# Kernel optimization log

Hardware: AMD Instinct MI355X
Metric: run time of the kernel (lower is better)

## Reference

```python
import jax, jax.numpy as jnp
import numpy as np

N, D, C = 8192, 1024, 1000
T_SCALE = 0.3
LAM2 = 0.1


def setup_inputs() -> dict:
    key = jax.random.key(0)
    k1, k2, k3 = jax.random.split(key, 3)
    feat = jax.random.normal(k1, (N, D), dtype=jnp.float32)
    W = jax.random.normal(k2, (C, D), dtype=jnp.float32) * 0.02
    b = jnp.zeros((C,), dtype=jnp.float32)
    labels = jax.random.randint(k3, (N,), 0, C)
    return {"feat": feat, "labels": labels, "W": W, "b": b}


def _scl_loss(feat_n, labels, t):
    # feat_n: l2-normalized features [N, D]
    n = feat_n.shape[0]
    sim = (feat_n @ feat_n.T) / t                      # [N, N]
    eye = jnp.eye(n, dtype=bool)
    # denominator: sum_{k != i} exp(sim[i,k])  (log-domain, same math)
    bottom_log = jax.nn.logsumexp(jnp.where(eye, -jnp.inf, sim), axis=1)  # [N]
    # positive mask: same label, j != i
    pos = (labels[:, None] == labels[None, :]) & ~eye  # [N, N]
    counts = pos.sum(axis=1)                           # [N]
    # log(exp(sim_ij)/bottom_i) = sim_ij - bottom_log_i
    sum_log = jnp.sum(jnp.where(pos, sim - bottom_log[:, None], 0.0), axis=1)
    valid = counts > 0
    per_sample = jnp.where(valid, -sum_log / jnp.maximum(counts, 1), 0.0)
    n_valid = valid.sum()
    return jnp.where(n_valid > 0, per_sample.sum() / jnp.maximum(n_valid, 1), 0.0)


def reference(feat, labels, W, b):
    logits = feat @ W.T + b                            # [N, C]
    # cross entropy (mean over batch)
    logp = jax.nn.log_softmax(logits, axis=-1)
    ce = -jnp.mean(jnp.take_along_axis(logp, labels[:, None], axis=1)[:, 0])
    # supervised contrastive loss on l2-normalized features
    feat_n = feat / jnp.linalg.norm(feat, axis=1, keepdims=True)
    scl = _scl_loss(feat_n, labels, T_SCALE)
    loss = (1.0 - LAM2) * ce + LAM2 * scl
    return logits, loss
```

## Files before the change

### kernel.cpp

```cpp
#include <hip/hip_runtime.h>
#include <hip/hip_bf16.h>
#include <math.h>

#define N 8192
#define D 1024
#define C 1000
#define CP 1024
#define INV_T (1.0f / 0.3f)
#define SIM_SCALE (INV_T / 256.0f)

typedef __bf16 bf16_t;
typedef bf16_t bf16x8 __attribute__((ext_vector_type(8)));
typedef float f32x4 __attribute__((ext_vector_type(4)));

typedef __attribute__((address_space(3))) uint32_t lds_u32_t;
typedef const __attribute__((address_space(1))) uint32_t glb_u32_t;

#define ZBYTES (3 * N * 4 + 16)
#define NZB 25

__global__ void prep_kernel(const float* __restrict__ feat,
                            const float* __restrict__ W,
                            float* __restrict__ norms, bf16_t* __restrict__ feat_n,
                            unsigned int* __restrict__ feat_f8,
                            bf16_t* __restrict__ Wp, char* __restrict__ zbase) {
  int g = blockIdx.x;
  int t = threadIdx.x;
  if (g < N) {
    int row = g;
    const float4* fr = (const float4*)(feat + (size_t)row * D);
    float4 x = fr[t];
    float ss = x.x * x.x + x.y * x.y + x.z * x.z + x.w * x.w;
    for (int off = 32; off; off >>= 1) ss += __shfl_down(ss, off, 64);
    __shared__ float sred[4];
    __shared__ float srn;
    int lane = t & 63, w = t >> 6;
    if (lane == 0) sred[w] = ss;
    __syncthreads();
    if (t == 0) {
      float tot = sred[0] + sred[1] + sred[2] + sred[3];
      float nrm = sqrtf(tot);
      norms[row] = nrm;
      srn = 1.0f / nrm;
    }
    __syncthreads();
    float rn = srn;
    union { bf16_t h[4]; uint2 u; } pk;
    pk.h[0] = (bf16_t)(x.x * rn);
    pk.h[1] = (bf16_t)(x.y * rn);
    pk.h[2] = (bf16_t)(x.z * rn);
    pk.h[3] = (bf16_t)(x.w * rn);
    *(uint2*)(feat_n + (size_t)row * D + t * 4) = pk.u;
    float rs = rn * 16.0f;
    unsigned int u8 = 0;
    u8 = __builtin_amdgcn_cvt_pk_fp8_f32(x.x * rs, x.y * rs, u8, false);
    u8 = __builtin_amdgcn_cvt_pk_fp8_f32(x.z * rs, x.w * rs, u8, true);
    feat_f8[(size_t)row * 256 + t] = u8;
  } else if (g < N + CP) {
    int row = g - N;
    union { bf16_t h[4]; uint2 u; } pk;
    if (row < C) {
      float4 x = ((const float4*)(W + (size_t)row * D))[t];
      pk.h[0] = (bf16_t)x.x; pk.h[1] = (bf16_t)x.y;
      pk.h[2] = (bf16_t)x.z; pk.h[3] = (bf16_t)x.w;
    } else {
      pk.h[0] = pk.h[1] = pk.h[2] = pk.h[3] = (bf16_t)0.0f;
    }
    *(uint2*)(Wp + (size_t)row * D + t * 4) = pk.u;
  } else {
    size_t off = (size_t)(g - N - CP) * 4096 + (size_t)t * 16;
    if (off < (size_t)ZBYTES) {
      int4 z = {0, 0, 0, 0};
      *(int4*)(zbase + off) = z;
    }
  }
}

#define BM 128
#define BN 128
#define BK 64
#define NSIM 2080

__device__ __forceinline__ void stage_tile_bf16(const bf16_t* __restrict__ g0,
                                                bf16_t* lds, int t, int w) {
#pragma unroll
  for (int p = 0; p < 4; p++) {
    int chunk = p * 256 + t;
    int r = chunk >> 3;
    int c = (chunk & 7) ^ (r & 7);
    const bf16_t* gp = g0 + (size_t)r * D + c * 8;
    bf16_t* lp = lds + (size_t)(p * 256 + w * 64) * 8;
    __builtin_amdgcn_global_load_lds((glb_u32_t*)gp, (lds_u32_t*)lp, 16, 0, 0);
  }
}

__device__ __forceinline__ void stage_tile_f8(const unsigned char* __restrict__ g0,
                                              unsigned char* lds, int t, int w) {
#pragma unroll
  for (int p = 0; p < 2; p++) {
    int chunk = p * 256 + t;
    int r = chunk >> 2;
    int c = (chunk & 3) ^ ((r >> 1) & 3);
    const unsigned char* gp = g0 + (size_t)r * D + c * 16;
    unsigned char* lp = lds + (size_t)(p * 256 + w * 64) * 16;
    __builtin_amdgcn_global_load_lds((glb_u32_t*)gp, (lds_u32_t*)lp, 16, 0, 0);
  }
}

__launch_bounds__(256)
__global__ void logits_gemm(const bf16_t* __restrict__ A, const bf16_t* __restrict__ Wp,
                            const float* __restrict__ norms, const float* __restrict__ bias,
                            float* __restrict__ ceS, float* __restrict__ out) {
  __shared__ __align__(16) bf16_t As[BM * BK];
  __shared__ __align__(16) bf16_t Bs[BN * BK];
  int tileM = blockIdx.x * BM;
  int tileN = blockIdx.y * BN;
  int t = threadIdx.x;
  int lane = t & 63;
  int w = t >> 6;
  int wm = (w & 1) << 6;
  int wn = (w >> 1) << 6;
  int l15 = lane & 15;
  int quad = lane >> 4;
  f32x4 acc[4][4] = {};
  const bf16_t* Abase = A + (size_t)tileM * D;
  const bf16_t* Bbase = Wp + (size_t)tileN * D;

  for (int k0 = 0; k0 < D; k0 += BK) {
    stage_tile_bf16(Abase + k0, As, t, w);
    stage_tile_bf16(Bbase + k0, Bs, t, w);
    __syncthreads();
#pragma unroll
    for (int h = 0; h < 2; h++) {
      bf16x8 af[4], bfr[4];
#pragma unroll
      for (int i = 0; i < 4; i++) {
        int ar = wm + i * 16 + l15;
        int cc = (h * 4 + quad) ^ (ar & 7);
        af[i] = *(const bf16x8*)(&As[ar * BK + cc * 8]);
      }
#pragma unroll
      for (int j = 0; j < 4; j++) {
        int br = wn + j * 16 + l15;
        int cc = (h * 4 + quad) ^ (br & 7);
        bfr[j] = *(const bf16x8*)(&Bs[br * BK + cc * 8]);
      }
#pragma unroll
      for (int i = 0; i < 4; i++)
#pragma unroll
        for (int j = 0; j < 4; j++)
          acc[i][j] = __builtin_amdgcn_mfma_f32_16x16x32_bf16(af[i], bfr[j], acc[i][j], 0, 0, 0);
    }
    __syncthreads();
  }
#pragma unroll
  for (int i = 0; i < 4; i++) {
#pragma unroll
    for (int r = 0; r < 4; r++) {
      int gr = tileM + wm + i * 16 + quad * 4 + r;
      float nrm = norms[gr];
      float esum = 0.0f;
#pragma unroll
      for (int j = 0; j < 4; j++) {
        int gc = tileN + wn + j * 16 + l15;
        if (gc < C) {
          float lg = nrm * acc[i][j][r] + bias[gc];
          out[(size_t)gr * C + gc] = lg;
          esum += __expf(lg);
        }
      }
      for (int m = 1; m < 16; m <<= 1) esum += __shfl_xor(esum, m, 64);
      if (l15 == 0) atomicAdd(&ceS[gr], esum);
    }
  }
}

__launch_bounds__(256)
__global__ void sim_gemm(const unsigned char* __restrict__ A8, const int* __restrict__ labels,
                         float* __restrict__ S, float* __restrict__ P) {
  __shared__ __align__(16) unsigned char As[BM * 64];
  __shared__ __align__(16) unsigned char Bs[BN * 64];
  int g = blockIdx.x;
  int t = threadIdx.x;
  int lane = t & 63;
  int w = t >> 6;
  int wm = (w & 1) << 6;
  int wn = (w >> 1) << 6;
  int l15 = lane & 15;
  int quad = lane >> 4;
  f32x4 acc[4][4] = {};

  const int nb = N / BM;
  float fnb = (float)nb + 0.5f;
  int bi = (int)(fnb - sqrtf(fnb * fnb - 2.0f * (float)g));
  if (bi < 0) bi = 0;
#define TRI_OFF(r) ((r) * nb - (r) * ((r)-1) / 2)
  while (TRI_OFF(bi + 1) <= g) bi++;
  while (TRI_OFF(bi) > g) bi--;
  int bj = bi + (g - TRI_OFF(bi));
#undef TRI_OFF
  bi = __builtin_amdgcn_readfirstlane(bi);
  bj = __builtin_amdgcn_readfirstlane(bj);
  int tileM = bi * BM;
  int tileN = bj * BN;
  bool diag = (bi == bj);

  const unsigned char* Abase = A8 + (size_t)tileM * D;
  const unsigned char* Bbase = A8 + (size_t)tileN * D;

  for (int k0 = 0; k0 < D; k0 += BK) {
    stage_tile_f8(Abase + k0, As, t, w);
    stage_tile_f8(Bbase + k0, Bs, t, w);
    __syncthreads();
#pragma unroll
    for (int h = 0; h < 2; h++) {
      long af[4], bfr[4];
#pragma unroll
      for (int i = 0; i < 4; i++) {
        int ar = wm + i * 16 + l15;
        int c8 = h * 4 + quad;
        int boff = ((c8 >> 1) ^ ((ar >> 1) & 3)) * 16 + (c8 & 1) * 8;
        af[i] = *(const long*)(&As[ar * 64 + boff]);
      }
#pragma unroll
      for (int j = 0; j < 4; j++) {
        int br = wn + j * 16 + l15;
        int c8 = h * 4 + quad;
        int boff = ((c8 >> 1) ^ ((br >> 1) & 3)) * 16 + (c8 & 1) * 8;
        bfr[j] = *(const long*)(&Bs[br * 64 + boff]);
      }
#pragma unroll
      for (int i = 0; i < 4; i++)
#pragma unroll
        for (int j = 0; j < 4; j++)
          acc[i][j] = __builtin_amdgcn_mfma_f32_16x16x32_fp8_fp8(af[i], bfr[j], acc[i][j], 0, 0, 0);
    }
    __syncthreads();
  }

  int gcj[4], lc[4];
#pragma unroll
  for (int j = 0; j < 4; j++) {
    gcj[j] = tileN + wn + j * 16 + l15;
    lc[j] = labels[gcj[j]];
  }
  float csS[4] = {0.f, 0.f, 0.f, 0.f}, csP[4] = {0.f, 0.f, 0.f, 0.f};
#pragma unroll
  for (int i = 0; i < 4; i++) {
#pragma unroll
    for (int r = 0; r < 4; r++) {
      int gr = tileM + wm + i * 16 + quad * 4 + r;
      int lr = labels[gr];
      float ssum = 0.0f, psum = 0.0f;
#pragma unroll
      for (int j = 0; j < 4; j++) {
        float sim = acc[i][j][r] * SIM_SCALE;
        if (gcj[j] != gr) {
          float e = __expf(sim);
          float pv = (lc[j] == lr) ? sim : 0.0f;
          ssum += e;
          psum += pv;
          csS[j] += e;
          csP[j] += pv;
        }
      }
      for (int m = 1; m < 16; m <<= 1) {
        ssum += __shfl_xor(ssum, m, 64);
        psum += __shfl_xor(psum, m, 64);
      }
      if (l15 == 0) {
        atomicAdd(&S[gr], ssum);
        atomicAdd(&P[gr], psum);
      }
    }
  }
  if (!diag) {
#pragma unroll
    for (int j = 0; j < 4; j++) {
      csS[j] += __shfl_xor(csS[j], 16, 64);
      csS[j] += __shfl_xor(csS[j], 32, 64);
      csP[j] += __shfl_xor(csP[j], 16, 64);
      csP[j] += __shfl_xor(csP[j], 32, 64);
      if (quad == 0) {
        atomicAdd(&S[gcj[j]], csS[j]);
        atomicAdd(&P[gcj[j]], csP[j]);
      }
    }
  }
}

__global__ void final_kernel(const float* __restrict__ S, const float* __restrict__ P,
                             const int* __restrict__ labels,
                             const float* __restrict__ ceS, float* __restrict__ out,
                             float* __restrict__ accums) {
  __shared__ int lh[1024];
  int t = threadIdx.x;
  for (int i = t; i < 1024; i += 256) lh[i] = 0;
  __syncthreads();
  for (int i = t; i < N; i += 256) atomicAdd(&lh[labels[i]], 1);
  __syncthreads();

  int i = blockIdx.x * 256 + t;
  int lab = labels[i];
  float cesum = logf(ceS[i]) - out[(size_t)i * C + lab];
  float lsum = 0.0f, lval = 0.0f;
  int cnt = lh[lab] - 1;
  if (cnt > 0) {
    float bl = logf(S[i]);
    lsum = -(P[i] - (float)cnt * bl) / (float)cnt;
    lval = 1.0f;
  }
  for (int off = 32; off; off >>= 1) {
    cesum += __shfl_down(cesum, off, 64);
    lsum += __shfl_down(lsum, off, 64);
    lval += __shfl_down(lval, off, 64);
  }
  __shared__ float sc[4], ss[4], sv[4];
  int lane = t & 63, w = t >> 6;
  if (lane == 0) { sc[w] = cesum; ss[w] = lsum; sv[w] = lval; }
  __syncthreads();
  if (t == 0) {
    atomicAdd(&accums[0], sc[0] + sc[1] + sc[2] + sc[3]);
    atomicAdd(&accums[1], ss[0] + ss[1] + ss[2] + ss[3]);
    atomicAdd(&accums[2], sv[0] + sv[1] + sv[2] + sv[3]);
    __threadfence();
    unsigned int prev = atomicAdd((unsigned int*)&accums[3], 1u);
    if (prev == 31) {
      float a0 = atomicAdd(&accums[0], 0.0f);
      float a1 = atomicAdd(&accums[1], 0.0f);
      float a2 = atomicAdd(&accums[2], 0.0f);
      float ce = a0 * (1.0f / (float)N);
      float scl = (a2 > 0.0f) ? a1 / a2 : 0.0f;
      out[(size_t)N * C] = 0.9f * ce + 0.1f * scl;
    }
  }
}

extern "C" void kernel_launch(void* const* d_in, const int* in_sizes, int n_in,
                              void* d_out, int out_size, void* d_ws, size_t ws_size,
                              hipStream_t stream) {
  const float* feat   = (const float*)d_in[0];
  const int*   labels = (const int*)d_in[1];
  const float* W      = (const float*)d_in[2];
  const float* b      = (const float*)d_in[3];
  float* out = (float*)d_out;

  char* ws = (char*)d_ws;
  bf16_t*       feat_n  = (bf16_t*)ws;
  bf16_t*       Wp      = (bf16_t*)(ws + (size_t)N * D * 2);
  unsigned int* feat_f8 = (unsigned int*)(ws + (size_t)N * D * 2 + (size_t)CP * D * 2);
  float*  norms  = (float*)((char*)feat_f8 + (size_t)N * D);
  float*  S      = norms + N;
  float*  P      = S + N;
  float*  ceS    = P + N;
  float*  accums = ceS + N;

  prep_kernel<<<N + CP + NZB, 256, 0, stream>>>(feat, W, norms, feat_n, feat_f8,
                                                Wp, (char*)S);
  logits_gemm<<<dim3(N / BM, CP / BN), 256, 0, stream>>>(feat_n, Wp, norms, b, ceS, out);
  sim_gemm<<<NSIM, 256, 0, stream>>>((const unsigned char*)feat_f8, labels, S, P);
  final_kernel<<<N / 256, 256, 0, stream>>>(S, P, labels, ceS, out, accums);
}
```

Baseline: 248.8 us.

## Switch sim GEMM to 32x32x64 scaled FP8 MFMA and cache labels in LDS

Replaces the 16x16x32 FP8 MFMA tiling in the similarity GEMM with the gfx950 32x32x64 scaled f8f6f4 MFMA (unit scales). Fragments become 32-byte reads and the epilogue is remapped to the 32x32 accumulator layout. Tile labels are now staged into LDS once instead of read from global memory per row. The aim is fewer MFMA issues and fewer LDS reads per K step. In exchange, the row reductions now need 5-step shuffles and the new output row mapping must be exactly right.

```diff
diff --git a/kernel.cpp b/kernel.cpp
--- a/kernel.cpp
+++ b/kernel.cpp
@@ -12,6 +12,9 @@
 typedef __bf16 bf16_t;
 typedef bf16_t bf16x8 __attribute__((ext_vector_type(8)));
 typedef float f32x4 __attribute__((ext_vector_type(4)));
+typedef float f32x16 __attribute__((ext_vector_type(16)));
+typedef int v8i __attribute__((ext_vector_type(8)));
+typedef int v4i __attribute__((ext_vector_type(4)));
 
 typedef __attribute__((address_space(3))) uint32_t lds_u32_t;
 typedef const __attribute__((address_space(1))) uint32_t glb_u32_t;
@@ -107,6 +110,13 @@
   }
 }
 
+__device__ __forceinline__ v8i read_frag_f8(const unsigned char* rowbase, int s, int kh) {
+  v8i r;
+  *(v4i*)&r         = *(const v4i*)(rowbase + (((2 * kh) ^ s) << 4));
+  *(((v4i*)&r) + 1) = *(const v4i*)(rowbase + (((2 * kh + 1) ^ s) << 4));
+  return r;
+}
+
 __launch_bounds__(256)
 __global__ void logits_gemm(const bf16_t* __restrict__ A, const bf16_t* __restrict__ Wp,
                             const float* __restrict__ norms, const float* __restrict__ bias,
@@ -180,15 +190,17 @@
                          float* __restrict__ S, float* __restrict__ P) {
   __shared__ __align__(16) unsigned char As[BM * 64];
   __shared__ __align__(16) unsigned char Bs[BN * 64];
+  __shared__ int lblA[BM];
+  __shared__ int lblB[BN];
   int g = blockIdx.x;
   int t = threadIdx.x;
   int lane = t & 63;
   int w = t >> 6;
   int wm = (w & 1) << 6;
   int wn = (w >> 1) << 6;
-  int l15 = lane & 15;
-  int quad = lane >> 4;
-  f32x4 acc[4][4] = {};
+  int l31 = lane & 31;
+  int kh = lane >> 5;
+  f32x16 acc[2][2] = {};
 
   const int nb = N / BM;
   float fnb = (float)nb + 0.5f;
@@ -205,6 +217,9 @@
   int tileN = bj * BN;
   bool diag = (bi == bj);
 
+  if (t < BM) lblA[t] = labels[tileM + t];
+  else lblB[t - BM] = labels[tileN + (t - BM)];
+
   const unsigned char* Abase = A8 + (size_t)tileM * D;
   const unsigned char* Bbase = A8 + (size_t)tileN * D;
 
@@ -212,63 +227,59 @@
     stage_tile_f8(Abase + k0, As, t, w);
     stage_tile_f8(Bbase + k0, Bs, t, w);
     __syncthreads();
-#pragma unroll
-    for (int h = 0; h < 2; h++) {
-      long af[4], bfr[4];
-#pragma unroll
-      for (int i = 0; i < 4; i++) {
-        int ar = wm + i * 16 + l15;
-        int c8 = h * 4 + quad;
-        int boff = ((c8 >> 1) ^ ((ar >> 1) & 3)) * 16 + (c8 & 1) * 8;
-        af[i] = *(const long*)(&As[ar * 64 + boff]);
-      }
-#pragma unroll
-      for (int j = 0; j < 4; j++) {
-        int br = wn + j * 16 + l15;
-        int c8 = h * 4 + quad;
-        int boff = ((c8 >> 1) ^ ((br >> 1) & 3)) * 16 + (c8 & 1) * 8;
-        bfr[j] = *(const long*)(&Bs[br * 64 + boff]);
-      }
-#pragma unroll
-      for (int i = 0; i < 4; i++)
-#pragma unroll
-        for (int j = 0; j < 4; j++)
-          acc[i][j] = __builtin_amdgcn_mfma_f32_16x16x32_fp8_fp8(af[i], bfr[j], acc[i][j], 0, 0, 0);
-    }
-    __syncthreads();
-  }
-
-  int gcj[4], lc[4];
-#pragma unroll
-  for (int j = 0; j < 4; j++) {
-    gcj[j] = tileN + wn + j * 16 + l15;
-    lc[j] = labels[gcj[j]];
-  }
-  float csS[4] = {0.f, 0.f, 0.f, 0.f}, csP[4] = {0.f, 0.f, 0.f, 0.f};
-#pragma unroll
-  for (int i = 0; i < 4; i++) {
-#pragma unroll
-    for (int r = 0; r < 4; r++) {
-      int gr = tileM + wm + i * 16 + quad * 4 + r;
-      int lr = labels[gr];
+    v8i af[2], bf[2];
+#pragma unroll
+    for (int i = 0; i < 2; i++) {
+      int ar = wm + i * 32 + l31;
+      af[i] = read_frag_f8(&As[ar * 64], (ar >> 1) & 3, kh);
+    }
+#pragma unroll
+    for (int j = 0; j < 2; j++) {
+      int br = wn + j * 32 + l31;
+      bf[j] = read_frag_f8(&Bs[br * 64], (br >> 1) & 3, kh);
+    }
+#pragma unroll
+    for (int i = 0; i < 2; i++)
+#pragma unroll
+      for (int j = 0; j < 2; j++)
+        acc[i][j] = __builtin_amdgcn_mfma_scale_f32_32x32x64_f8f6f4(
+            af[i], bf[j], acc[i][j], 0, 0,
+            0, 0x7f7f7f7f, 0, 0x7f7f7f7f);
+    __syncthreads();
+  }
+
+  int gcj[2], lcj[2];
+#pragma unroll
+  for (int j = 0; j < 2; j++) {
+    gcj[j] = tileN + wn + j * 32 + l31;
+    lcj[j] = lblB[wn + j * 32 + l31];
+  }
+  float csS[2] = {0.f, 0.f}, csP[2] = {0.f, 0.f};
+#pragma unroll
+  for (int i = 0; i < 2; i++) {
+#pragma unroll
+    for (int reg = 0; reg < 16; reg++) {
+      int rrow = (reg & 3) + 8 * (reg >> 2) + 4 * kh;
+      int gr = tileM + wm + i * 32 + rrow;
+      int lr = lblA[wm + i * 32 + rrow];
       float ssum = 0.0f, psum = 0.0f;
 #pragma unroll
-      for (int j = 0; j < 4; j++) {
-        float sim = acc[i][j][r] * SIM_SCALE;
+      for (int j = 0; j < 2; j++) {
+        float sim = acc[i][j][reg] * SIM_SCALE;
         if (gcj[j] != gr) {
           float e = __expf(sim);
-          float pv = (lc[j] == lr) ? sim : 0.0f;
+          float pv = (lcj[j] == lr) ? sim : 0.0f;
           ssum += e;
           psum += pv;
           csS[j] += e;
           csP[j] += pv;
         }
       }
-      for (int m = 1; m < 16; m <<= 1) {
+      for (int m = 1; m < 32; m <<= 1) {
         ssum += __shfl_xor(ssum, m, 64);
         psum += __shfl_xor(psum, m, 64);
       }
-      if (l15 == 0) {
+      if (l31 == 0) {
         atomicAdd(&S[gr], ssum);
         atomicAdd(&P[gr], psum);
       }
@@ -276,12 +287,10 @@
   }
   if (!diag) {
 #pragma unroll
-    for (int j = 0; j < 4; j++) {
-      csS[j] += __shfl_xor(csS[j], 16, 64);
+    for (int j = 0; j < 2; j++) {
       csS[j] += __shfl_xor(csS[j], 32, 64);
-      csP[j] += __shfl_xor(csP[j], 16, 64);
       csP[j] += __shfl_xor(csP[j], 32, 64);
-      if (quad == 0) {
+      if (kh == 0) {
         atomicAdd(&S[gcj[j]], csS[j]);
         atomicAdd(&P[gcj[j]], csP[j]);
       }
```

Result: slower. 386.1 us (+55.2%).
